# Kernel optimization log

Hardware: AMD Instinct MI355X
Metric: run time of the kernel (lower is better)

The kernel has to match this reference:

```python
import jax, jax.numpy as jnp
import numpy as np

D_MODEL = 64

def setup_inputs() -> dict:
    key = jax.random.key(0)
    k1, k2, k3, k4 = jax.random.split(key, 4)
    B, T, E = 4, 4096, 128
    x = jax.random.normal(k1, (B, T, E), dtype=jnp.float32)
    # nn.Linear weights, stored transposed as (in, out) for x @ W
    s = 1.0 / np.sqrt(E)
    Wq = jax.random.uniform(k2, (E, D_MODEL), jnp.float32, -s, s)
    Wk = jax.random.uniform(k3, (E, D_MODEL), jnp.float32, -s, s)
    Wv = jax.random.uniform(k4, (E, D_MODEL), jnp.float32, -s, s)
    return {"x": x, "Wq": Wq, "Wk": Wk, "Wv": Wv}

def reference(x, Wq, Wk, Wv):
    B, T, E = x.shape
    q = jnp.einsum('bte,ed->btd', x, Wq)
    k = jnp.einsum('bte,ed->btd', x, Wk)
    v = jnp.einsum('bte,ed->btd', x, Wv)
    scores = jnp.einsum('bqd,bkd->bqk', q, k) / np.sqrt(D_MODEL)  # [B,T,T]
    causal = jnp.tril(jnp.ones((T, T), dtype=bool))
    scores = jnp.where(causal, scores, jnp.float32(-1e9))
    attn = jax.nn.softmax(scores, axis=-1)
    # dropout p=0.0 -> identity (eval-mode faithful)
    return jnp.einsum('bqk,bkd->bqd', attn, v)
```

## Files before the change

kernel.cpp:

```cpp
#include <hip/hip_runtime.h>
#include <hip/hip_bf16.h>


typedef __attribute__((ext_vector_type(4))) float  f32x4;
typedef __attribute__((ext_vector_type(4))) unsigned int u32x4;
typedef __attribute__((ext_vector_type(8))) __bf16 bf16x8;
typedef __attribute__((ext_vector_type(8))) unsigned short u16x8;
typedef __attribute__((ext_vector_type(4))) unsigned short u16x4;

#define T_SEQ 4096
#define DH    64
#define EDIM  128
#define KVB   64
#define QSCALE 0.18033688f
#define NTRI  528

__device__ __forceinline__ unsigned short f2bf(float f) {
    unsigned int x = __builtin_bit_cast(unsigned int, f);
    unsigned int r = x + 0x7fffu + ((x >> 16) & 1u);
    return (unsigned short)(r >> 16);
}

__device__ __forceinline__ unsigned int cvt_pk_bf16(float lo, float hi) {
    unsigned int d;
    asm("v_cvt_pk_bf16_f32 %0, %1, %2" : "=v"(d) : "v"(lo), "v"(hi));
    return d;
}

__device__ __forceinline__ f32x4 mfma_bf16(u16x8 a, u16x8 b, f32x4 c) {
    return __builtin_amdgcn_mfma_f32_16x16x32_bf16(
        __builtin_bit_cast(bf16x8, a), __builtin_bit_cast(bf16x8, b), c, 0, 0, 0);
}

__device__ __forceinline__ int kswz(int row, int bcol) {
    return row * 128 + (bcol ^ ((row & 7) << 4));
}
__device__ __forceinline__ int vswz(int row, int bcol) {
    return row * 256 + (bcol ^ ((row & 15) << 4));
}

__global__ __launch_bounds__(256) void prep_w_kernel(
    const float* __restrict__ wq, const float* __restrict__ wk,
    const float* __restrict__ wv, unsigned short* __restrict__ wt)
{
    int o = blockIdx.x * 256 + threadIdx.x;
    int m   = o >> 13;
    int rem = o & 8191;
    int d = rem >> 7, e = rem & 127;
    const float* W = (m == 0) ? wq : (m == 1) ? wk : wv;
    wt[o] = f2bf(W[e * DH + d]);
}

__global__ __launch_bounds__(64) void proj_kernel(
    const float* __restrict__ x, const unsigned short* __restrict__ wt,
    unsigned short* __restrict__ qw, unsigned short* __restrict__ kw,
    unsigned short* __restrict__ vt)
{
    const int l   = threadIdx.x;
    const int l15 = l & 15;
    const int lg  = l >> 4;
    const int row0 = blockIdx.x * 16;
    const int b    = row0 >> 12;
    const int t0   = row0 & 4095;

    u16x8 af[4];
    #pragma unroll
    for (int kt = 0; kt < 4; ++kt) {
        const float* xp = x + (row0 + l15) * EDIM + kt * 32 + lg * 8;
        f32x4 a = *(const f32x4*)xp;
        f32x4 bb = *(const f32x4*)(xp + 4);
        af[kt] = u16x8{ f2bf(a[0]), f2bf(a[1]), f2bf(a[2]), f2bf(a[3]),
                        f2bf(bb[0]), f2bf(bb[1]), f2bf(bb[2]), f2bf(bb[3]) };
    }

    unsigned short* outs[2] = { qw, kw };
    #pragma unroll
    for (int m = 0; m < 2; ++m) {
        #pragma unroll
        for (int nt = 0; nt < 4; ++nt) {
            f32x4 acc = {};
            #pragma unroll
            for (int kt = 0; kt < 4; ++kt) {
                u16x8 bfrag = *(const u16x8*)(wt + (m * 64 + nt * 16 + l15) * EDIM
                                                 + kt * 32 + lg * 8);
                acc = mfma_bf16(af[kt], bfrag, acc);
            }
            const float sc = (m == 0) ? QSCALE : 1.0f;
            #pragma unroll
            for (int r = 0; r < 4; ++r)
                outs[m][(row0 + lg * 4 + r) * DH + nt * 16 + l15] = f2bf(acc[r] * sc);
        }
    }

    #pragma unroll
    for (int nt = 0; nt < 4; ++nt) {
        f32x4 acc = {};
        #pragma unroll
        for (int kt = 0; kt < 4; ++kt) {
            u16x8 bfrag = *(const u16x8*)(wt + (2 * 64 + nt * 16 + l15) * EDIM
                                             + kt * 32 + lg * 8);
            acc = mfma_bf16(af[kt], bfrag, acc);
        }
        u16x4 pv = { f2bf(acc[0]), f2bf(acc[1]), f2bf(acc[2]), f2bf(acc[3]) };
        *(u16x4*)(vt + ((size_t)(b * DH + nt * 16 + l15)) * T_SEQ + t0 + lg * 4) = pv;
    }
}

__global__ __launch_bounds__(256, 4) void attn_partial_kernel(
    const unsigned short* __restrict__ qg, const unsigned short* __restrict__ kg,
    const unsigned short* __restrict__ vt,
    unsigned short* __restrict__ po, float* __restrict__ pm, float* __restrict__ pl)
{
    const int phys = blockIdx.x;
    const int bid  = (phys & 7) * 264 + (phys >> 3);
    const int b   = bid / NTRI;
    const int i   = bid - b * NTRI;
    int q = (int)((__builtin_sqrtf((float)(8 * i + 1)) - 1.0f) * 0.5f);
    while (q * (q + 1) / 2 > i) --q;
    while ((q + 1) * (q + 2) / 2 <= i) ++q;
    const int q128 = q;
    const int ch   = i - q * (q + 1) / 2;

    __shared__ char K_ldsb[128 * 128];
    __shared__ char V_ldsb[64 * 256];

    const int tid = threadIdx.x;
    const int w   = tid >> 6;
    const int l   = tid & 63;
    const int l15 = l & 15;
    const int lg  = l >> 4;

    const int base   = b * T_SEQ;
    const int qrow0w = q128 * 128 + w * 32;
    const int kvb    = ch * 128;

    const unsigned short* kgB = kg + (size_t)base * DH;
    const unsigned short* vtB = vt + (size_t)b * DH * T_SEQ;

    {
        u16x8 kr[4], vr[4];
        #pragma unroll
        for (int j = 0; j < 4; ++j) {
            int gi = tid + j * 256;
            kr[j] = *(const u16x8*)(kgB + (size_t)(kvb + (gi >> 3)) * DH + (gi & 7) * 8);
            vr[j] = *(const u16x8*)(vtB + (size_t)(gi >> 4) * T_SEQ + kvb + (gi & 15) * 8);
        }
        #pragma unroll
        for (int j = 0; j < 4; ++j) {
            int gi = tid + j * 256;
            *(u16x8*)&K_ldsb[kswz(gi >> 3, (gi & 7) * 16)]  = kr[j];
            *(u16x8*)&V_ldsb[vswz(gi >> 4, (gi & 15) * 16)] = vr[j];
        }
    }

    u16x8 qf[2][2];
    #pragma unroll
    for (int rt = 0; rt < 2; ++rt) {
        const unsigned short* qrow = qg + (base + qrow0w + rt * 16 + l15) * DH;
        qf[rt][0] = *(const u16x8*)(qrow + 0 + lg * 8);
        qf[rt][1] = *(const u16x8*)(qrow + 32 + lg * 8);
    }

    f32x4 o_acc[2][4];
    float m_run[2], l_run[2];
    #pragma unroll
    for (int rt = 0; rt < 2; ++rt) {
        #pragma unroll
        for (int dt = 0; dt < 4; ++dt) o_acc[rt][dt] = f32x4{};
        m_run[rt] = -1e30f; l_run[rt] = 0.0f;
    }

    const int src0 = l15 + 32 * (lg & 1);
    const int src1 = src0 + 16;
    const bool hi  = (lg >> 1) != 0;

    __syncthreads();

    #pragma unroll
    for (int tt = 0; tt < 2; ++tt) {
        const int kv0 = kvb + tt * 64;
        if (kv0 > qrow0w + 31) continue;

        u16x8 kf[4][2];
        #pragma unroll
        for (int nt = 0; nt < 4; ++nt)
            #pragma unroll
            for (int kt = 0; kt < 2; ++kt) {
                int krow = tt * 64 + nt * 16 + l15;
                kf[nt][kt] = *(const u16x8*)&K_ldsb[kswz(krow, kt * 64 + lg * 16)];
            }

        f32x4 s[2][4];
        __builtin_amdgcn_s_setprio(1);
        #pragma unroll
        for (int rt = 0; rt < 2; ++rt)
            #pragma unroll
            for (int nt = 0; nt < 4; ++nt) {
                f32x4 a = {};
                a = mfma_bf16(kf[nt][0], qf[rt][0], a);
                a = mfma_bf16(kf[nt][1], qf[rt][1], a);
                s[rt][nt] = a;
            }
        __builtin_amdgcn_s_setprio(0);

        if (kv0 + KVB - 1 > qrow0w) {
            #pragma unroll
            for (int rt = 0; rt < 2; ++rt)
                #pragma unroll
                for (int nt = 0; nt < 4; ++nt)
                    #pragma unroll
                    for (int rr = 0; rr < 4; ++rr) {
                        int kj = kv0 + nt * 16 + lg * 4 + rr;
                        int qi = qrow0w + rt * 16 + l15;
                        if (kj > qi) s[rt][nt][rr] = -1e30f;
                    }
        }

        float sc2[2];
        bool grow = false;
        unsigned int pk[2][4][2];
        #pragma unroll
        for (int rt = 0; rt < 2; ++rt) {
            float mx = s[rt][0][0];
            #pragma unroll
            for (int nt = 0; nt < 4; ++nt)
                #pragma unroll
                for (int rr = 0; rr < 4; ++rr)
                    mx = fmaxf(mx, s[rt][nt][rr]);
            mx = fmaxf(mx, __shfl_xor(mx, 16));
            mx = fmaxf(mx, __shfl_xor(mx, 32));

            float mold = m_run[rt];
            float mnew = fmaxf(mold, mx);
            grow |= (mx > mold);
            float sc = exp2f(mold - mnew);
            sc2[rt] = sc;
            m_run[rt] = mnew;

            float rs = 0.0f;
            #pragma unroll
            for (int nt = 0; nt < 4; ++nt)
                #pragma unroll
                for (int rr = 0; rr < 4; ++rr) {
                    float p = exp2f(s[rt][nt][rr] - mnew);
                    s[rt][nt][rr] = p;
                    rs += p;
                }
            rs += __shfl_xor(rs, 16);
            rs += __shfl_xor(rs, 32);
            l_run[rt] = l_run[rt] * sc + rs;

            #pragma unroll
            for (int nt = 0; nt < 4; ++nt) {
                pk[rt][nt][0] = cvt_pk_bf16(s[rt][nt][0], s[rt][nt][1]);
                pk[rt][nt][1] = cvt_pk_bf16(s[rt][nt][2], s[rt][nt][3]);
            }
        }
        if (__any(grow)) {
            #pragma unroll
            for (int rt = 0; rt < 2; ++rt)
                #pragma unroll
                for (int dt = 0; dt < 4; ++dt)
                    o_acc[rt][dt] *= sc2[rt];
        }

        __builtin_amdgcn_s_setprio(1);
        #pragma unroll
        for (int kt = 0; kt < 2; ++kt) {
            u16x8 vf[4];
            #pragma unroll
            for (int dt = 0; dt < 4; ++dt) {
                int vrow = dt * 16 + l15;
                vf[dt] = *(const u16x8*)&V_ldsb[vswz(vrow, tt * 128 + kt * 64 + lg * 16)];
            }
            #pragma unroll
            for (int rt = 0; rt < 2; ++rt) {
                unsigned int pb[4];
                #pragma unroll
                for (int t = 0; t < 4; ++t) {
                    int src = (t < 2) ? src0 : src1;
                    unsigned int pa  = __shfl(pk[rt][2 * kt][t & 1], src);
                    unsigned int pbv = __shfl(pk[rt][2 * kt + 1][t & 1], src);
                    pb[t] = hi ? pbv : pa;
                }
                u32x4 pbq = { pb[0], pb[1], pb[2], pb[3] };
                u16x8 pbf = __builtin_bit_cast(u16x8, pbq);
                #pragma unroll
                for (int dt = 0; dt < 4; ++dt)
                    o_acc[rt][dt] = mfma_bf16(vf[dt], pbf, o_acc[rt][dt]);
            }
        }
        __builtin_amdgcn_s_setprio(0);
    }

    const int pidx = bid;
    unsigned short* pob = po + (size_t)pidx * 8192;
    #pragma unroll
    for (int rt = 0; rt < 2; ++rt) {
        int row = w * 32 + rt * 16 + l15;
        #pragma unroll
        for (int dt = 0; dt < 4; ++dt) {
            unsigned int w0 = cvt_pk_bf16(o_acc[rt][dt][0], o_acc[rt][dt][1]);
            unsigned int w1 = cvt_pk_bf16(o_acc[rt][dt][2], o_acc[rt][dt][3]);
            *(unsigned int*)&pob[row * 64 + dt * 16 + lg * 4]     = w0;
            *(unsigned int*)&pob[row * 64 + dt * 16 + lg * 4 + 2] = w1;
        }
        if (lg == 0) {
            pm[pidx * 128 + row] = m_run[rt];
            pl[pidx * 128 + row] = l_run[rt];
        }
    }
}

__global__ __launch_bounds__(256) void attn_combine_kernel(
    const unsigned short* __restrict__ po, const float* __restrict__ pm,
    const float* __restrict__ pl, float* __restrict__ out)
{
    const int blk   = blockIdx.x;
    const int slice = blk & 3;
    const int tb    = blk >> 2;
    const int q128  = tb & 31;
    const int b     = tb >> 5;
    const int nch   = q128 + 1;
    const int bslot = b * NTRI + q128 * (q128 + 1) / 2;
    const int row   = slice * 32 + (threadIdx.x >> 3);
    const int d0    = (threadIdx.x & 7) * 8;

    float m_i[32];
    #pragma unroll
    for (int i = 0; i < 32; ++i) {
        int ii = (i < nch) ? i : 0;
        m_i[i] = pm[(bslot + ii) * 128 + row];
    }
    float mstar = m_i[0];
    #pragma unroll
    for (int i = 1; i < 32; ++i)
        if (i < nch) mstar = fmaxf(mstar, m_i[i]);

    float lsum = 0.0f;
    float a[8] = {};
    #pragma unroll
    for (int i = 0; i < 32; ++i) {
        if (i < nch) {
            float wi = exp2f(m_i[i] - mstar);
            lsum += wi * pl[(bslot + i) * 128 + row];
            u16x8 v = *(const u16x8*)&po[(size_t)(bslot + i) * 8192 + row * 64 + d0];
            #pragma unroll
            for (int j = 0; j < 8; ++j) {
                unsigned int u = (unsigned int)v[j] << 16;
                a[j] += wi * __builtin_bit_cast(float, u);
            }
        }
    }
    const float inv = 1.0f / lsum;
    float* op = out + (size_t)(b * T_SEQ + q128 * 128 + row) * DH + d0;
    f32x4 o0 = { a[0] * inv, a[1] * inv, a[2] * inv, a[3] * inv };
    f32x4 o1 = { a[4] * inv, a[5] * inv, a[6] * inv, a[7] * inv };
    *(f32x4*)op = o0;
    *(f32x4*)(op + 4) = o1;
}

__global__ __launch_bounds__(64, 4) void attn_direct_kernel(
    const unsigned short* __restrict__ qg, const unsigned short* __restrict__ kg,
    const unsigned short* __restrict__ vt, float* __restrict__ out)
{
    const int bid = blockIdx.x;
    const int q32 = bid & 127;
    const int b   = bid >> 7;
    const int l = threadIdx.x, l15 = l & 15, lg = l >> 4;
    const int qrow0 = q32 * 32;
    const int base  = b * T_SEQ;
    const unsigned short* kp = kg + (size_t)base * DH;
    const unsigned short* vp = vt + (size_t)b * DH * T_SEQ;

    u16x8 qf[2][2];
    #pragma unroll
    for (int rt = 0; rt < 2; ++rt) {
        const unsigned short* qrow = qg + (base + qrow0 + rt * 16 + l15) * DH;
        qf[rt][0] = *(const u16x8*)(qrow + 0 + lg * 8);
        qf[rt][1] = *(const u16x8*)(qrow + 32 + lg * 8);
    }

    f32x4 o_acc[2][4];
    float m_run[2], l_run[2];
    #pragma unroll
    for (int rt = 0; rt < 2; ++rt) {
        #pragma unroll
        for (int dt = 0; dt < 4; ++dt) o_acc[rt][dt] = f32x4{};
        m_run[rt] = -1e30f; l_run[rt] = 0.0f;
    }

    const int src0 = l15 + 32 * (lg & 1);
    const int src1 = src0 + 16;
    const bool hi  = (lg >> 1) != 0;

    for (int kv0 = 0; kv0 <= qrow0 + 31; kv0 += KVB) {
        u16x8 kf[4][2];
        #pragma unroll
        for (int nt = 0; nt < 4; ++nt)
            #pragma unroll
            for (int kt = 0; kt < 2; ++kt)
                kf[nt][kt] = *(const u16x8*)(kp + (kv0 + nt * 16 + l15) * DH
                                                + kt * 32 + lg * 8);
        f32x4 s[2][4];
        #pragma unroll
        for (int rt = 0; rt < 2; ++rt)
            #pragma unroll
            for (int nt = 0; nt < 4; ++nt) {
                f32x4 a = {};
                a = mfma_bf16(kf[nt][0], qf[rt][0], a);
                a = mfma_bf16(kf[nt][1], qf[rt][1], a);
                s[rt][nt] = a;
            }
        if (kv0 + KVB - 1 > qrow0) {
            #pragma unroll
            for (int rt = 0; rt < 2; ++rt)
                #pragma unroll
                for (int nt = 0; nt < 4; ++nt)
                    #pragma unroll
                    for (int rr = 0; rr < 4; ++rr) {
                        int kj = kv0 + nt * 16 + lg * 4 + rr;
                        int qi = qrow0 + rt * 16 + l15;
                        if (kj > qi) s[rt][nt][rr] = -1e30f;
                    }
        }
        float sc2[2];
        bool grow = false;
        unsigned int pk[2][4][2];
        #pragma unroll
        for (int rt = 0; rt < 2; ++rt) {
            float mx = s[rt][0][0];
            #pragma unroll
            for (int nt = 0; nt < 4; ++nt)
                #pragma unroll
                for (int rr = 0; rr < 4; ++rr)
                    mx = fmaxf(mx, s[rt][nt][rr]);
            mx = fmaxf(mx, __shfl_xor(mx, 16));
            mx = fmaxf(mx, __shfl_xor(mx, 32));
            float mold = m_run[rt];
            float mnew = fmaxf(mold, mx);
            grow |= (mx > mold);
            float sc = exp2f(mold - mnew);
            sc2[rt] = sc;
            m_run[rt] = mnew;
            float rs = 0.0f;
            #pragma unroll
            for (int nt = 0; nt < 4; ++nt)
                #pragma unroll
                for (int rr = 0; rr < 4; ++rr) {
                    float p = exp2f(s[rt][nt][rr] - mnew);
                    s[rt][nt][rr] = p;
                    rs += p;
                }
            rs += __shfl_xor(rs, 16);
            rs += __shfl_xor(rs, 32);
            l_run[rt] = l_run[rt] * sc + rs;
            #pragma unroll
            for (int nt = 0; nt < 4; ++nt) {
                pk[rt][nt][0] = cvt_pk_bf16(s[rt][nt][0], s[rt][nt][1]);
                pk[rt][nt][1] = cvt_pk_bf16(s[rt][nt][2], s[rt][nt][3]);
            }
        }
        if (__any(grow)) {
            #pragma unroll
            for (int rt = 0; rt < 2; ++rt)
                #pragma unroll
                for (int dt = 0; dt < 4; ++dt)
                    o_acc[rt][dt] *= sc2[rt];
        }
        #pragma unroll
        for (int kt = 0; kt < 2; ++kt) {
            u16x8 vf[4];
            #pragma unroll
            for (int dt = 0; dt < 4; ++dt)
                vf[dt] = *(const u16x8*)(vp + (size_t)(dt * 16 + l15) * T_SEQ
                                            + kv0 + kt * 32 + lg * 8);
            #pragma unroll
            for (int rt = 0; rt < 2; ++rt) {
                unsigned int pb[4];
                #pragma unroll
                for (int t = 0; t < 4; ++t) {
                    int src = (t < 2) ? src0 : src1;
                    unsigned int pa  = __shfl(pk[rt][2 * kt][t & 1], src);
                    unsigned int pbv = __shfl(pk[rt][2 * kt + 1][t & 1], src);
                    pb[t] = hi ? pbv : pa;
                }
                u32x4 pbq = { pb[0], pb[1], pb[2], pb[3] };
                u16x8 pbf = __builtin_bit_cast(u16x8, pbq);
                #pragma unroll
                for (int dt = 0; dt < 4; ++dt)
                    o_acc[rt][dt] = mfma_bf16(vf[dt], pbf, o_acc[rt][dt]);
            }
        }
    }

    #pragma unroll
    for (int rt = 0; rt < 2; ++rt) {
        float inv = 1.0f / l_run[rt];
        int row = base + qrow0 + rt * 16 + l15;
        #pragma unroll
        for (int dt = 0; dt < 4; ++dt) {
            f32x4 ov = o_acc[rt][dt] * inv;
            *(f32x4*)&out[(size_t)row * DH + dt * 16 + lg * 4] = ov;
        }
    }
}

extern "C" void kernel_launch(void* const* d_in, const int* in_sizes, int n_in,
                              void* d_out, int out_size, void* d_ws, size_t ws_size,
                              hipStream_t stream)
{
    const float* x  = (const float*)d_in[0];
    const float* wq = (const float*)d_in[1];
    const float* wk = (const float*)d_in[2];
    const float* wv = (const float*)d_in[3];
    float* out = (float*)d_out;

    unsigned short* wt = (unsigned short*)d_ws;
    unsigned short* qw = (unsigned short*)((char*)d_ws + 65536);
    unsigned short* kw = qw + (size_t)16384 * DH;
    unsigned short* vt = kw + (size_t)16384 * DH;

    const size_t slots  = 4u * NTRI;
    const size_t po_off = 65536u + 3u * 16384u * DH * 2u;
    const size_t po_sz  = slots * 8192 * 2;
    const size_t pm_off = po_off + po_sz;
    const size_t pl_off = pm_off + slots * 128 * 4;
    const size_t need   = pl_off + slots * 128 * 4;

    prep_w_kernel<<<96, 256, 0, stream>>>(wq, wk, wv, wt);
    proj_kernel<<<1024, 64, 0, stream>>>(x, wt, qw, kw, vt);

    if (ws_size >= need) {
        unsigned short* po = (unsigned short*)((char*)d_ws + po_off);
        float* pm = (float*)((char*)d_ws + pm_off);
        float* pl = (float*)((char*)d_ws + pl_off);
        attn_partial_kernel<<<4 * NTRI, 256, 0, stream>>>(qw, kw, vt, po, pm, pl);
        attn_combine_kernel<<<4 * 32 * 4, 256, 0, stream>>>(po, pm, pl, out);
    } else {
        attn_direct_kernel<<<4 * 128, 64, 0, stream>>>(qw, kw, vt, out);
    }
}
```

Measured before the change: 60.08 us.

## Compute softmax over full 128-key chunk at once, dropping online rescaling

```diff
diff --git a/kernel.cpp b/kernel.cpp
--- a/kernel.cpp
+++ b/kernel.cpp
@@ -106,7 +106,7 @@
     }
 }
 
-__global__ __launch_bounds__(256, 4) void attn_partial_kernel(
+__global__ __launch_bounds__(256, 3) void attn_partial_kernel(
     const unsigned short* __restrict__ qg, const unsigned short* __restrict__ kg,
     const unsigned short* __restrict__ vt,
     unsigned short* __restrict__ po, float* __restrict__ pm, float* __restrict__ pl)
@@ -162,13 +162,10 @@
     }
 
     f32x4 o_acc[2][4];
-    float m_run[2], l_run[2];
-    #pragma unroll
-    for (int rt = 0; rt < 2; ++rt) {
+    #pragma unroll
+    for (int rt = 0; rt < 2; ++rt)
         #pragma unroll
         for (int dt = 0; dt < 4; ++dt) o_acc[rt][dt] = f32x4{};
-        m_run[rt] = -1e30f; l_run[rt] = 0.0f;
-    }
 
     const int src0 = l15 + 32 * (lg & 1);
     const int src1 = src0 + 16;
@@ -176,122 +173,109 @@
 
     __syncthreads();
 
-    #pragma unroll
-    for (int tt = 0; tt < 2; ++tt) {
-        const int kv0 = kvb + tt * 64;
-        if (kv0 > qrow0w + 31) continue;
-
-        u16x8 kf[4][2];
-        #pragma unroll
-        for (int nt = 0; nt < 4; ++nt)
-            #pragma unroll
-            for (int kt = 0; kt < 2; ++kt) {
-                int krow = tt * 64 + nt * 16 + l15;
-                kf[nt][kt] = *(const u16x8*)&K_ldsb[kswz(krow, kt * 64 + lg * 16)];
-            }
-
-        f32x4 s[2][4];
+    const bool t1        = (kvb + 64 <= qrow0w + 31);
+    const bool need_mask = (kvb + 127 > qrow0w);
+
+    float msv[2], lsv[2];
+    unsigned int pk2[2][8][2];
+
+    #pragma unroll
+    for (int rt = 0; rt < 2; ++rt) {
+        f32x4 s[8];
+        #pragma unroll
+        for (int nt = 0; nt < 8; ++nt)
+            s[nt] = f32x4{ -1e30f, -1e30f, -1e30f, -1e30f };
+
         __builtin_amdgcn_s_setprio(1);
         #pragma unroll
-        for (int rt = 0; rt < 2; ++rt)
+        for (int nt = 0; nt < 4; ++nt) {
+            int krow = nt * 16 + l15;
+            u16x8 k0 = *(const u16x8*)&K_ldsb[kswz(krow, 0 + lg * 16)];
+            u16x8 k1 = *(const u16x8*)&K_ldsb[kswz(krow, 64 + lg * 16)];
+            f32x4 a = {};
+            a = mfma_bf16(k0, qf[rt][0], a);
+            a = mfma_bf16(k1, qf[rt][1], a);
+            s[nt] = a;
+        }
+        if (t1) {
             #pragma unroll
             for (int nt = 0; nt < 4; ++nt) {
+                int krow = 64 + nt * 16 + l15;
+                u16x8 k0 = *(const u16x8*)&K_ldsb[kswz(krow, 0 + lg * 16)];
+                u16x8 k1 = *(const u16x8*)&K_ldsb[kswz(krow, 64 + lg * 16)];
                 f32x4 a = {};
-                a = mfma_bf16(kf[nt][0], qf[rt][0], a);
-                a = mfma_bf16(kf[nt][1], qf[rt][1], a);
-                s[rt][nt] = a;
-            }
+                a = mfma_bf16(k0, qf[rt][0], a);
+                a = mfma_bf16(k1, qf[rt][1], a);
+                s[4 + nt] = a;
+            }
+        }
         __builtin_amdgcn_s_setprio(0);
 
-        if (kv0 + KVB - 1 > qrow0w) {
-            #pragma unroll
-            for (int rt = 0; rt < 2; ++rt)
-                #pragma unroll
-                for (int nt = 0; nt < 4; ++nt)
-                    #pragma unroll
-                    for (int rr = 0; rr < 4; ++rr) {
-                        int kj = kv0 + nt * 16 + lg * 4 + rr;
-                        int qi = qrow0w + rt * 16 + l15;
-                        if (kj > qi) s[rt][nt][rr] = -1e30f;
-                    }
-        }
-
-        float sc2[2];
-        bool grow = false;
-        unsigned int pk[2][4][2];
+        if (need_mask) {
+            const int qi = qrow0w + rt * 16 + l15;
+            #pragma unroll
+            for (int nt = 0; nt < 8; ++nt)
+                #pragma unroll
+                for (int rr = 0; rr < 4; ++rr) {
+                    int kj = kvb + nt * 16 + lg * 4 + rr;
+                    if (kj > qi) s[nt][rr] = -1e30f;
+                }
+        }
+
+        float mx = s[0][0];
+        #pragma unroll
+        for (int nt = 0; nt < 8; ++nt)
+            #pragma unroll
+            for (int rr = 0; rr < 4; ++rr)
+                mx = fmaxf(mx, s[nt][rr]);
+        mx = fmaxf(mx, __shfl_xor(mx, 16));
+        mx = fmaxf(mx, __shfl_xor(mx, 32));
+
+        float rs = 0.0f;
+        #pragma unroll
+        for (int nt = 0; nt < 8; ++nt) {
+            float e0 = exp2f(s[nt][0] - mx);
+            float e1 = exp2f(s[nt][1] - mx);
+            float e2 = exp2f(s[nt][2] - mx);
+            float e3 = exp2f(s[nt][3] - mx);
+            rs += (e0 + e1) + (e2 + e3);
+            pk2[rt][nt][0] = cvt_pk_bf16(e0, e1);
+            pk2[rt][nt][1] = cvt_pk_bf16(e2, e3);
+        }
+        rs += __shfl_xor(rs, 16);
+        rs += __shfl_xor(rs, 32);
+        msv[rt] = mx;
+        lsv[rt] = rs;
+    }
+
+    __builtin_amdgcn_s_setprio(1);
+    #pragma unroll
+    for (int kt = 0; kt < 4; ++kt) {
+        if (kt >= 2 && !t1) continue;
+        u16x8 vf[4];
+        #pragma unroll
+        for (int dt = 0; dt < 4; ++dt) {
+            int vrow = dt * 16 + l15;
+            vf[dt] = *(const u16x8*)&V_ldsb[vswz(vrow, kt * 64 + lg * 16)];
+        }
         #pragma unroll
         for (int rt = 0; rt < 2; ++rt) {
-            float mx = s[rt][0][0];
-            #pragma unroll
-            for (int nt = 0; nt < 4; ++nt)
-                #pragma unroll
-                for (int rr = 0; rr < 4; ++rr)
-                    mx = fmaxf(mx, s[rt][nt][rr]);
-            mx = fmaxf(mx, __shfl_xor(mx, 16));
-            mx = fmaxf(mx, __shfl_xor(mx, 32));
-
-            float mold = m_run[rt];
-            float mnew = fmaxf(mold, mx);
-            grow |= (mx > mold);
-            float sc = exp2f(mold - mnew);
-            sc2[rt] = sc;
-            m_run[rt] = mnew;
-
-            float rs = 0.0f;
-            #pragma unroll
-            for (int nt = 0; nt < 4; ++nt)
-                #pragma unroll
-                for (int rr = 0; rr < 4; ++rr) {
-                    float p = exp2f(s[rt][nt][rr] - mnew);
-                    s[rt][nt][rr] = p;
-                    rs += p;
-                }
-            rs += __shfl_xor(rs, 16);
-            rs += __shfl_xor(rs, 32);
-            l_run[rt] = l_run[rt] * sc + rs;
-
-            #pragma unroll
-            for (int nt = 0; nt < 4; ++nt) {
-                pk[rt][nt][0] = cvt_pk_bf16(s[rt][nt][0], s[rt][nt][1]);
-                pk[rt][nt][1] = cvt_pk_bf16(s[rt][nt][2], s[rt][nt][3]);
-            }
-        }
-        if (__any(grow)) {
-            #pragma unroll
-            for (int rt = 0; rt < 2; ++rt)
-                #pragma unroll
-                for (int dt = 0; dt < 4; ++dt)
-                    o_acc[rt][dt] *= sc2[rt];
-        }
-
-        __builtin_amdgcn_s_setprio(1);
-        #pragma unroll
-        for (int kt = 0; kt < 2; ++kt) {
-            u16x8 vf[4];
-            #pragma unroll
-            for (int dt = 0; dt < 4; ++dt) {
-                int vrow = dt * 16 + l15;
-                vf[dt] = *(const u16x8*)&V_ldsb[vswz(vrow, tt * 128 + kt * 64 + lg * 16)];
-            }
-            #pragma unroll
-            for (int rt = 0; rt < 2; ++rt) {
-                unsigned int pb[4];
-                #pragma unroll
-                for (int t = 0; t < 4; ++t) {
-                    int src = (t < 2) ? src0 : src1;
-                    unsigned int pa  = __shfl(pk[rt][2 * kt][t & 1], src);
-                    unsigned int pbv = __shfl(pk[rt][2 * kt + 1][t & 1], src);
-                    pb[t] = hi ? pbv : pa;
-                }
-                u32x4 pbq = { pb[0], pb[1], pb[2], pb[3] };
-                u16x8 pbf = __builtin_bit_cast(u16x8, pbq);
-                #pragma unroll
-                for (int dt = 0; dt < 4; ++dt)
-                    o_acc[rt][dt] = mfma_bf16(vf[dt], pbf, o_acc[rt][dt]);
-            }
-        }
-        __builtin_amdgcn_s_setprio(0);
-    }
+            unsigned int pb[4];
+            #pragma unroll
+            for (int t = 0; t < 4; ++t) {
+                int src = (t < 2) ? src0 : src1;
+                unsigned int pa  = __shfl(pk2[rt][2 * kt][t & 1], src);
+                unsigned int pbv = __shfl(pk2[rt][2 * kt + 1][t & 1], src);
+                pb[t] = hi ? pbv : pa;
+            }
+            u32x4 pbq = { pb[0], pb[1], pb[2], pb[3] };
+            u16x8 pbf = __builtin_bit_cast(u16x8, pbq);
+            #pragma unroll
+            for (int dt = 0; dt < 4; ++dt)
+                o_acc[rt][dt] = mfma_bf16(vf[dt], pbf, o_acc[rt][dt]);
+        }
+    }
+    __builtin_amdgcn_s_setprio(0);
 
     const int pidx = bid;
     unsigned short* pob = po + (size_t)pidx * 8192;
@@ -306,8 +290,8 @@
             *(unsigned int*)&pob[row * 64 + dt * 16 + lg * 4 + 2] = w1;
         }
         if (lg == 0) {
-            pm[pidx * 128 + row] = m_run[rt];
-            pl[pidx * 128 + row] = l_run[rt];
+            pm[pidx * 128 + row] = msv[rt];
+            pl[pidx * 128 + row] = lsv[rt];
         }
     }
 }
```

After: 58.88 us (median of 3 runs). -2.0%, faster.
